# Optimization experiments

Measured on AMD Instinct MI355X. Metric: run time of the kernel, lower is better.

Reference implementation:

```python
import jax, jax.numpy as jnp
import numpy as np

BATCH = 32768


def _unpack(packed, n):
    # packed: [rows, ceil(n/8)] ints in [0,256). Extract bits MSB-first per byte.
    bits = (packed[:, :, None] >> jnp.arange(7, -1, -1, dtype=packed.dtype)) & 1
    return bits.reshape(packed.shape[0], -1)[:, :n]  # [rows, n] of {0,1}


def setup_inputs() -> dict:
    key = jax.random.key(0)
    k0, k1, k2, k3, k4 = jax.random.split(key, 5)
    return {
        "x": jax.random.normal(k0, (BATCH, 784), dtype=jnp.float32),
        "w1_packed": jax.random.randint(k1, (256, 98), 0, 256, dtype=jnp.int32),
        "m1_packed": jax.random.randint(k2, (256, 98), 0, 256, dtype=jnp.int32),
        "alpha1": jnp.float32(1.0),
        "w2_packed": jax.random.randint(k3, (10, 32), 0, 256, dtype=jnp.int32),
        "m2_packed": jax.random.randint(k4, (10, 32), 0, 256, dtype=jnp.int32),
        "alpha2": jnp.float32(1.0),
    }


def reference(x, w1_packed, m1_packed, alpha1, w2_packed, m2_packed, alpha2):
    # Layer 1: binary {-1,+1} weights * {0,1} mask * alpha
    w1 = (2 * _unpack(w1_packed, 784) - 1).astype(jnp.float32)
    w1 = w1 * _unpack(m1_packed, 784).astype(jnp.float32) * alpha1  # [256, 784]
    h = jax.nn.relu(jnp.einsum('bi,oi->bo', x, w1))  # [B, 256]
    # Layer 2
    w2 = (2 * _unpack(w2_packed, 256) - 1).astype(jnp.float32)
    w2 = w2 * _unpack(m2_packed, 256).astype(jnp.float32) * alpha2  # [10, 256]
    return jnp.einsum('bh,oh->bo', h, w2)  # [B, 10]
```

## Files before the change

kernel.cpp:

```cpp
#include <hip/hip_runtime.h>
#include <hip/hip_bf16.h>

typedef __bf16 bf16x8 __attribute__((ext_vector_type(8)));
typedef float floatx4 __attribute__((ext_vector_type(4)));

__device__ __forceinline__ unsigned short f2bf(float f) {
  __bf16 b = (__bf16)f;
  return __builtin_bit_cast(unsigned short, b);
}

__global__ void decode_w1_kernel(const int* __restrict__ w1p,
                                 const int* __restrict__ m1p,
                                 unsigned short* __restrict__ w1t) {
  int t = blockIdx.x * 256 + threadIdx.x;
  int r = t & 255;
  int j = t >> 8;
  unsigned short vals[8];
#pragma unroll
  for (int k = 0; k < 8; ++k) vals[k] = 0;
  if (j < 98) {
    unsigned int v = (unsigned int)w1p[r * 98 + j];
    unsigned int m = (unsigned int)m1p[r * 98 + j];
#pragma unroll
    for (int k = 0; k < 8; ++k) {
      unsigned int bit = (v >> (7 - k)) & 1u;
      unsigned int mk  = (m >> (7 - k)) & 1u;
      vals[k] = (unsigned short)(mk ? (bit ? 0x3F80u : 0xBF80u) : 0u);
    }
  }
  uint4 pack;
  pack.x = (unsigned)vals[0] | ((unsigned)vals[1] << 16);
  pack.y = (unsigned)vals[2] | ((unsigned)vals[3] << 16);
  pack.z = (unsigned)vals[4] | ((unsigned)vals[5] << 16);
  pack.w = (unsigned)vals[6] | ((unsigned)vals[7] << 16);
  *reinterpret_cast<uint4*>(w1t + t * 8) = pack;
}

#define BM 32
#define NCHG 26
#define HS_LD 264
#define W2_LD 264

#define OFF_W2 8448

__global__ __launch_bounds__(512, 4) void fused_kernel(
    const float* __restrict__ x,
    const unsigned short* __restrict__ w1t,
    const int* __restrict__ w2p,
    const int* __restrict__ m2p,
    const float* __restrict__ a1p,
    const float* __restrict__ a2p,
    float* __restrict__ out) {
  __shared__ unsigned short smem[26624];

  const int tid  = threadIdx.x;
  const int wave = tid >> 6;
  const int lane = tid & 63;
  const int l15  = lane & 15;
  const int quad = lane >> 4;
  const int row0 = blockIdx.x * BM;

  {
    const int r  = tid >> 4;
    const int g0 = tid & 15;
    float4 xv[13];
#pragma unroll
    for (int it = 0; it < 13; ++it) {
      int g = g0 + it * 16;
      int col = g * 4;
      if (col < 784)
        xv[it] = *reinterpret_cast<const float4*>(
            x + (size_t)(row0 + r) * 784 + col);
      else
        xv[it] = (float4){0.f, 0.f, 0.f, 0.f};
    }
#pragma unroll
    for (int it = 0; it < 13; ++it) {
      int g = g0 + it * 16;
      ushort4 b;
      b.x = f2bf(xv[it].x); b.y = f2bf(xv[it].y);
      b.z = f2bf(xv[it].z); b.w = f2bf(xv[it].w);
      *reinterpret_cast<ushort4*>(&smem[(g >> 1) * 256 + r * 8 + (g & 1) * 4]) = b;
    }
  }
  __syncthreads();

  floatx4 acc[2][2];
#pragma unroll
  for (int i = 0; i < 2; ++i)
#pragma unroll
    for (int j = 0; j < 2; ++j) acc[i][j] = (floatx4){0.f, 0.f, 0.f, 0.f};

  const unsigned short* wl = w1t + ((size_t)wave * 32 + l15) * 8;

#pragma unroll
  for (int cl = 0; cl < NCHG; ++cl) {
    bf16x8 af[2], bfv[2];
#pragma unroll
    for (int mi = 0; mi < 2; ++mi)
      af[mi] = *reinterpret_cast<const bf16x8*>(
          &smem[(cl * 4 + quad) * 256 + (mi * 16 + l15) * 8]);
#pragma unroll
    for (int nj = 0; nj < 2; ++nj)
      bfv[nj] = *reinterpret_cast<const bf16x8*>(
          wl + (size_t)(cl * 4 + quad) * 2048 + nj * 128);
#pragma unroll
    for (int mi = 0; mi < 2; ++mi)
#pragma unroll
      for (int nj = 0; nj < 2; ++nj)
        acc[mi][nj] = __builtin_amdgcn_mfma_f32_16x16x32_bf16(
            af[mi], bfv[nj], acc[mi][nj], 0, 0, 0);
  }
  __syncthreads();

  const float a1 = a1p[0];
  const float a2 = a2p[0];
#pragma unroll
  for (int mi = 0; mi < 2; ++mi) {
#pragma unroll
    for (int nj = 0; nj < 2; ++nj) {
      int col   = wave * 32 + nj * 16 + l15;
      int rbase = mi * 16 + quad * 4;
#pragma unroll
      for (int r = 0; r < 4; ++r) {
        float h = fmaxf(a1 * acc[mi][nj][r], 0.f);
        smem[(rbase + r) * HS_LD + col] = f2bf(h);
      }
    }
  }
  if (tid < 320) {
    int r = tid >> 5, j = tid & 31;
    unsigned int v = (unsigned int)w2p[r * 32 + j];
    unsigned int m = (unsigned int)m2p[r * 32 + j];
#pragma unroll
    for (int k = 0; k < 8; ++k) {
      unsigned int bit = (v >> (7 - k)) & 1u;
      unsigned int mk  = (m >> (7 - k)) & 1u;
      smem[OFF_W2 + r * W2_LD + j * 8 + k] =
          (unsigned short)(mk ? (bit ? 0x3F80u : 0xBF80u) : 0u);
    }
  }
  for (int idx = tid; idx < 6 * 256; idx += 512) {
    int r = 10 + (idx >> 8), c = idx & 255;
    smem[OFF_W2 + r * W2_LD + c] = 0;
  }
  __syncthreads();

  if (wave < 2) {
    floatx4 o2 = (floatx4){0.f, 0.f, 0.f, 0.f};
#pragma unroll
    for (int ks = 0; ks < 8; ++ks) {
      bf16x8 ha = *reinterpret_cast<const bf16x8*>(
          &smem[(wave * 16 + l15) * HS_LD + ks * 32 + quad * 8]);
      bf16x8 wb = *reinterpret_cast<const bf16x8*>(
          &smem[OFF_W2 + l15 * W2_LD + ks * 32 + quad * 8]);
      o2 = __builtin_amdgcn_mfma_f32_16x16x32_bf16(ha, wb, o2, 0, 0, 0);
    }
    if (l15 < 10) {
#pragma unroll
      for (int r = 0; r < 4; ++r) {
        int gr = row0 + wave * 16 + quad * 4 + r;
        out[(size_t)gr * 10 + l15] = a2 * o2[r];
      }
    }
  }
}

extern "C" void kernel_launch(void* const* d_in, const int* in_sizes, int n_in,
                              void* d_out, int out_size, void* d_ws, size_t ws_size,
                              hipStream_t stream) {
  const float* x   = (const float*)d_in[0];
  const int*   w1p = (const int*)d_in[1];
  const int*   m1p = (const int*)d_in[2];
  const float* a1  = (const float*)d_in[3];
  const int*   w2p = (const int*)d_in[4];
  const int*   m2p = (const int*)d_in[5];
  const float* a2  = (const float*)d_in[6];
  unsigned short* w1t = (unsigned short*)d_ws;
  float* out = (float*)d_out;

  decode_w1_kernel<<<104, 256, 0, stream>>>(w1p, m1p, w1t);
  fused_kernel<<<1024, 512, 0, stream>>>(x, w1t, w2p, m2p, a1, a2, out);
}
```

Before: 172.4 us.

## Stage x tile in two halves to halve LDS and raise occupancy

Splits the x staging and layer-1 MFMA loop into two halves of 13 chunks each, reusing a half-sized LDS buffer (about 26 KB instead of 52 KB). The launch bound moves to 8 blocks per CU so more blocks can stay resident to hide global load latency. The cost is two extra block-wide barriers, and the second half's x loads are serialized behind the first half's compute. Register pressure for the x staging also drops, from 13 to 7 float4 per thread.

```diff
diff --git a/kernel.cpp b/kernel.cpp
--- a/kernel.cpp
+++ b/kernel.cpp
@@ -37,13 +37,12 @@
 }
 
 #define BM 32
-#define NCHG 26
 #define HS_LD 264
 #define W2_LD 264
 
 #define OFF_W2 8448
 
-__global__ __launch_bounds__(512, 4) void fused_kernel(
+__global__ __launch_bounds__(512, 8) void fused_kernel(
     const float* __restrict__ x,
     const unsigned short* __restrict__ w1t,
     const int* __restrict__ w2p,
@@ -51,7 +50,7 @@
     const float* __restrict__ a1p,
     const float* __restrict__ a2p,
     float* __restrict__ out) {
-  __shared__ unsigned short smem[26624];
+  __shared__ unsigned short smem[13312];
 
   const int tid  = threadIdx.x;
   const int wave = tid >> 6;
@@ -60,57 +59,70 @@
   const int quad = lane >> 4;
   const int row0 = blockIdx.x * BM;
 
-  {
-    const int r  = tid >> 4;
-    const int g0 = tid & 15;
-    float4 xv[13];
-#pragma unroll
-    for (int it = 0; it < 13; ++it) {
-      int g = g0 + it * 16;
-      int col = g * 4;
-      if (col < 784)
-        xv[it] = *reinterpret_cast<const float4*>(
-            x + (size_t)(row0 + r) * 784 + col);
-      else
-        xv[it] = (float4){0.f, 0.f, 0.f, 0.f};
-    }
-#pragma unroll
-    for (int it = 0; it < 13; ++it) {
-      int g = g0 + it * 16;
-      ushort4 b;
-      b.x = f2bf(xv[it].x); b.y = f2bf(xv[it].y);
-      b.z = f2bf(xv[it].z); b.w = f2bf(xv[it].w);
-      *reinterpret_cast<ushort4*>(&smem[(g >> 1) * 256 + r * 8 + (g & 1) * 4]) = b;
-    }
-  }
-  __syncthreads();
-
   floatx4 acc[2][2];
 #pragma unroll
   for (int i = 0; i < 2; ++i)
 #pragma unroll
     for (int j = 0; j < 2; ++j) acc[i][j] = (floatx4){0.f, 0.f, 0.f, 0.f};
 
+  const int sr = tid >> 4;
+  const int g0 = tid & 15;
+  const float* xrow = x + (size_t)(row0 + sr) * 784;
+
+  auto stage_half = [&](int sp) {
+    float4 xv[7];
+#pragma unroll
+    for (int it = 0; it < 7; ++it) {
+      int g = g0 + it * 16;
+      int col = sp * 416 + g * 4;
+      if (g < 104 && col < 784)
+        xv[it] = *reinterpret_cast<const float4*>(xrow + col);
+      else
+        xv[it] = (float4){0.f, 0.f, 0.f, 0.f};
+    }
+#pragma unroll
+    for (int it = 0; it < 7; ++it) {
+      int g = g0 + it * 16;
+      if (g < 104) {
+        ushort4 b;
+        b.x = f2bf(xv[it].x); b.y = f2bf(xv[it].y);
+        b.z = f2bf(xv[it].z); b.w = f2bf(xv[it].w);
+        *reinterpret_cast<ushort4*>(&smem[(g >> 1) * 256 + sr * 8 + (g & 1) * 4]) = b;
+      }
+    }
+  };
+
   const unsigned short* wl = w1t + ((size_t)wave * 32 + l15) * 8;
 
+  auto compute_half = [&](int hb) {
 #pragma unroll
-  for (int cl = 0; cl < NCHG; ++cl) {
-    bf16x8 af[2], bfv[2];
-#pragma unroll
-    for (int mi = 0; mi < 2; ++mi)
-      af[mi] = *reinterpret_cast<const bf16x8*>(
-          &smem[(cl * 4 + quad) * 256 + (mi * 16 + l15) * 8]);
-#pragma unroll
-    for (int nj = 0; nj < 2; ++nj)
-      bfv[nj] = *reinterpret_cast<const bf16x8*>(
-          wl + (size_t)(cl * 4 + quad) * 2048 + nj * 128);
-#pragma unroll
-    for (int mi = 0; mi < 2; ++mi)
+    for (int cl = 0; cl < 13; ++cl) {
+      const int cg = hb * 13 + cl;
+      bf16x8 af[2], bfv[2];
 #pragma unroll
       for (int nj = 0; nj < 2; ++nj)
-        acc[mi][nj] = __builtin_amdgcn_mfma_f32_16x16x32_bf16(
-            af[mi], bfv[nj], acc[mi][nj], 0, 0, 0);
-  }
+        bfv[nj] = *reinterpret_cast<const bf16x8*>(
+            wl + (size_t)(cg * 4 + quad) * 2048 + nj * 128);
+#pragma unroll
+      for (int mi = 0; mi < 2; ++mi)
+        af[mi] = *reinterpret_cast<const bf16x8*>(
+            &smem[(cl * 4 + quad) * 256 + (mi * 16 + l15) * 8]);
+#pragma unroll
+      for (int mi = 0; mi < 2; ++mi)
+#pragma unroll
+        for (int nj = 0; nj < 2; ++nj)
+          acc[mi][nj] = __builtin_amdgcn_mfma_f32_16x16x32_bf16(
+              af[mi], bfv[nj], acc[mi][nj], 0, 0, 0);
+    }
+  };
+
+  stage_half(0);
+  __syncthreads();
+  compute_half(0);
+  __syncthreads();
+  stage_half(1);
+  __syncthreads();
+  compute_half(1);
   __syncthreads();
 
   const float a1 = a1p[0];
@@ -122,27 +134,27 @@
       int col   = wave * 32 + nj * 16 + l15;
       int rbase = mi * 16 + quad * 4;
 #pragma unroll
-      for (int r = 0; r < 4; ++r) {
-        float h = fmaxf(a1 * acc[mi][nj][r], 0.f);
-        smem[(rbase + r) * HS_LD + col] = f2bf(h);
+      for (int rr = 0; rr < 4; ++rr) {
+        float h = fmaxf(a1 * acc[mi][nj][rr], 0.f);
+        smem[(rbase + rr) * HS_LD + col] = f2bf(h);
       }
     }
   }
   if (tid < 320) {
-    int r = tid >> 5, j = tid & 31;
-    unsigned int v = (unsigned int)w2p[r * 32 + j];
-    unsigned int m = (unsigned int)m2p[r * 32 + j];
+    int rr = tid >> 5, j = tid & 31;
+    unsigned int v = (unsigned int)w2p[rr * 32 + j];
+    unsigned int m = (unsigned int)m2p[rr * 32 + j];
 #pragma unroll
     for (int k = 0; k < 8; ++k) {
       unsigned int bit = (v >> (7 - k)) & 1u;
       unsigned int mk  = (m >> (7 - k)) & 1u;
-      smem[OFF_W2 + r * W2_LD + j * 8 + k] =
+      smem[OFF_W2 + rr * W2_LD + j * 8 + k] =
           (unsigned short)(mk ? (bit ? 0x3F80u : 0xBF80u) : 0u);
     }
   }
   for (int idx = tid; idx < 6 * 256; idx += 512) {
-    int r = 10 + (idx >> 8), c = idx & 255;
-    smem[OFF_W2 + r * W2_LD + c] = 0;
+    int rr = 10 + (idx >> 8), c = idx & 255;
+    smem[OFF_W2 + rr * W2_LD + c] = 0;
   }
   __syncthreads();
 
@@ -158,9 +170,9 @@
     }
     if (l15 < 10) {
 #pragma unroll
-      for (int r = 0; r < 4; ++r) {
-        int gr = row0 + wave * 16 + quad * 4 + r;
-        out[(size_t)gr * 10 + l15] = a2 * o2[r];
+      for (int rr = 0; rr < 4; ++rr) {
+        int gr = row0 + wave * 16 + quad * 4 + rr;
+        out[(size_t)gr * 10 + l15] = a2 * o2[rr];
       }
     }
   }
```

New measurement: 176.3 us. 2.3% more time.
